# Kernel tuning notes

Measured on AMD Instinct MI355X. Metric: run time of the kernel, lower is better.

Reference implementation:

```python
import jax, jax.numpy as jnp
import numpy as np

N = 10000
IN_DIM = 1024
HID = 128
LAT = 64
E = 320000


def setup_inputs() -> dict:
    key = jax.random.key(0)
    ks = jax.random.split(key, 12)
    def glorot(k, shape):
        lim = float(np.sqrt(6.0 / (shape[0] + shape[1])))
        return jax.random.uniform(k, shape, jnp.float32, -lim, lim)
    x = jax.random.normal(ks[0], (N, IN_DIM), jnp.float32)
    edge_index = jax.random.randint(ks[1], (2, E), 0, N, jnp.int64)
    return {
        "x": x,
        "edge_index": edge_index,
        "W_enc1": glorot(ks[2], (IN_DIM, HID)), "b_enc1": jnp.zeros((HID,), jnp.float32),
        "W_enc2": glorot(ks[3], (HID, LAT)),   "b_enc2": jnp.zeros((LAT,), jnp.float32),
        "W_att1": glorot(ks[4], (LAT, HID)),   "b_att1": jnp.zeros((HID,), jnp.float32),
        "W_att2": glorot(ks[5], (HID, IN_DIM)),"b_att2": jnp.zeros((IN_DIM,), jnp.float32),
        "W_str":  glorot(ks[6], (LAT, LAT)),   "b_str":  jnp.zeros((LAT,), jnp.float32),
    }


def _gcn_norm(edge_index, n):
    # PyG GCNConv default: add self-loops, symmetric normalization
    loop = jnp.arange(n, dtype=edge_index.dtype)
    send = jnp.concatenate([edge_index[0], loop])
    recv = jnp.concatenate([edge_index[1], loop])
    deg = jax.ops.segment_sum(jnp.ones_like(recv, dtype=jnp.float32), recv, num_segments=n)
    dis = jnp.where(deg > 0, jax.lax.rsqrt(deg), 0.0)
    norm = dis[send] * dis[recv]  # [E+N]
    return send, recv, norm


def _gcn(x, W, b, send, recv, norm, n):
    h = x @ W                                  # [N, out]
    msg = h[send] * norm[:, None]              # gather + scale
    agg = jax.ops.segment_sum(msg, recv, num_segments=n)  # scatter-add
    return agg + b


def reference(x, edge_index, W_enc1, b_enc1, W_enc2, b_enc2,
              W_att1, b_att1, W_att2, b_att2, W_str, b_str):
    n = x.shape[0]
    send, recv, norm = _gcn_norm(edge_index, n)
    # encoder
    h = jax.nn.relu(_gcn(x, W_enc1, b_enc1, send, recv, norm, n))
    z = jax.nn.relu(_gcn(h, W_enc2, b_enc2, send, recv, norm, n))
    # attribute decoder
    a = jax.nn.relu(_gcn(z, W_att1, b_att1, send, recv, norm, n))
    attr_recon = jax.nn.relu(_gcn(a, W_att2, b_att2, send, recv, norm, n))
    # structure decoder
    s = jax.nn.relu(_gcn(z, W_str, b_str, send, recv, norm, n))
    struct_recon = s @ s.T  # [N, N]
    return (attr_recon, struct_recon, z)
```

## Files before the change

### kernel.cpp

```cpp
#include <hip/hip_runtime.h>
#include <hip/hip_bf16.h>

#define IN_DIM 1024
#define HID 128
#define LAT 64
#define DEGPAD 128

typedef __attribute__((ext_vector_type(8))) short bf16x8;
typedef __attribute__((ext_vector_type(4))) short bf16x4;
typedef __attribute__((ext_vector_type(4))) float f32x4;


__global__ __launch_bounds__(256) void k_initcur(int* cursor, int n) {
    int i = blockIdx.x * 256 + threadIdx.x;
    if (i < n) cursor[i] = 0;
}

__global__ __launch_bounds__(256) void k_fillpad(const int* __restrict__ ei, int* cursor,
                                                 int* __restrict__ colPad, int E) {
    int e = blockIdx.x * 256 + threadIdx.x;
    if (e >= E) return;
    int s = ei[e], r = ei[E + e];
    int slot = atomicAdd(&cursor[r], 1);
    if (slot < DEGPAD) colPad[(size_t)r * DEGPAD + slot] = s;
}

__global__ __launch_bounds__(256) void k_dis(const int* __restrict__ cursor, float* dis, int n) {
    int i = blockIdx.x * 256 + threadIdx.x;
    if (i < n) dis[i] = rsqrtf((float)(cursor[i] + 1));
}


#define W1T_OFF 0
#define W2T_OFF 131072
#define Wa1T_OFF 139264
#define Wa2T_OFF 147456
#define WsT_OFF 278528
#define WT_TOTAL 282624

__global__ __launch_bounds__(256) void k_wsplit(const float* __restrict__ W1, const float* __restrict__ W2,
                                                const float* __restrict__ Wa1, const float* __restrict__ Wa2,
                                                const float* __restrict__ Ws,
                                                __hip_bfloat16* __restrict__ hi, __hip_bfloat16* __restrict__ lo) {
    int idx = blockIdx.x * 256 + threadIdx.x;
    if (idx >= WT_TOTAL) return;
    const float* src; int base, shK, Nc;
    if (idx < W2T_OFF)       { src = W1;  base = W1T_OFF;  shK = 10; Nc = 128; }
    else if (idx < Wa1T_OFF) { src = W2;  base = W2T_OFF;  shK = 7;  Nc = 64; }
    else if (idx < Wa2T_OFF) { src = Wa1; base = Wa1T_OFF; shK = 6;  Nc = 128; }
    else if (idx < WsT_OFF)  { src = Wa2; base = Wa2T_OFF; shK = 7;  Nc = 1024; }
    else                     { src = Ws;  base = WsT_OFF;  shK = 6;  Nc = 64; }
    int local = idx - base;
    int nn = local >> shK;
    int k = local & ((1 << shK) - 1);
    float v = src[(size_t)k * Nc + nn];
    __hip_bfloat16 h = __float2bfloat16(v);
    hi[idx] = h;
    lo[idx] = __float2bfloat16(v - __bfloat162float(h));
}


template<int F, bool BIAS, bool RELU, int OMODE>
__global__ __launch_bounds__(256) void k_spmm(const float* __restrict__ Hin,
                                              const int* __restrict__ colPad,
                                              const int* __restrict__ cursor,
                                              const float* __restrict__ dis,
                                              const float* __restrict__ bias,
                                              float* __restrict__ out, float* __restrict__ out2,
                                              __hip_bfloat16* __restrict__ ohi,
                                              __hip_bfloat16* __restrict__ olo, int n) {
    int wave = (blockIdx.x * 256 + threadIdx.x) >> 6;
    int lane = threadIdx.x & 63;
    if (wave >= n) return;
    int d = cursor[wave];
    if (d > DEGPAD) d = DEGPAD;
    const int* cp = colPad + (size_t)wave * DEGPAD;
    float acc[F / 64];
    const float* self = Hin + (size_t)wave * F;
#pragma unroll
    for (int j = 0; j < F / 64; ++j) acc[j] = self[lane + 64 * j];
    for (int p = 0; p < d; ++p) {
        int c = cp[p];
        const float* row = Hin + (size_t)c * F;
#pragma unroll
        for (int j = 0; j < F / 64; ++j) acc[j] += row[lane + 64 * j];
    }
    float di = dis[wave];
#pragma unroll
    for (int j = 0; j < F / 64; ++j) {
        float r = acc[j] * di;
        if (BIAS) r += bias[lane + 64 * j];
        if (RELU) r = fmaxf(r, 0.f);
        size_t idx = (size_t)wave * F + lane + 64 * j;
        if constexpr (OMODE == 1) {
            __hip_bfloat16 h = __float2bfloat16(r);
            ohi[idx] = h;
            olo[idx] = __float2bfloat16(r - __bfloat162float(h));
        } else {
            out[idx] = r;
            if constexpr (OMODE == 2) out2[idx] = r * di;
        }
    }
}


template<int AMODE, bool BIAS, bool RELU, bool DIS, bool SPLITOUT, bool NT>
__global__ __launch_bounds__(256) void k_gemm_mfma(
        const __hip_bfloat16* __restrict__ Ahi, const __hip_bfloat16* __restrict__ Alo,
        const float* __restrict__ Af,
        const __hip_bfloat16* __restrict__ Bthi, const __hip_bfloat16* __restrict__ Btlo,
        const float* __restrict__ bias, const float* __restrict__ dis,
        float* __restrict__ Cf, __hip_bfloat16* __restrict__ Chi, __hip_bfloat16* __restrict__ Clo,
        int M, int K, int Nc) {
    __shared__ float tile[128 * 68];
    int tid = threadIdx.x;
    int w = tid >> 6, lane = tid & 63;
    int wr = w >> 1, wc = w & 1;
    int m0 = blockIdx.y * 128, n0 = blockIdx.x * 64;
    int lrow = lane & 15, lk = (lane >> 4) * 8;

    int arow[4];
    size_t aoff[4];
#pragma unroll
    for (int mi = 0; mi < 4; ++mi) {
        arow[mi] = m0 + wr * 64 + mi * 16 + lrow;
        aoff[mi] = (size_t)arow[mi] * K + lk;
    }
    size_t boff[2];
#pragma unroll
    for (int nj = 0; nj < 2; ++nj)
        boff[nj] = (size_t)(n0 + wc * 32 + nj * 16 + lrow) * K + lk;

    f32x4 acc[4][2] = {};

    for (int k0 = 0; k0 < K; k0 += 32) {
        bf16x8 bh[2], bl[2], ah[4], al[4];
#pragma unroll
        for (int nj = 0; nj < 2; ++nj) {
            bh[nj] = *(const bf16x8*)(Bthi + boff[nj] + k0);
            bl[nj] = *(const bf16x8*)(Btlo + boff[nj] + k0);
        }
        if constexpr (AMODE == 0) {
#pragma unroll
            for (int mi = 0; mi < 4; ++mi) {
                ah[mi] = *(const bf16x8*)(Ahi + aoff[mi] + k0);
                al[mi] = *(const bf16x8*)(Alo + aoff[mi] + k0);
            }
        } else {
#pragma unroll
            for (int mi = 0; mi < 4; ++mi) {
                float4 f0 = make_float4(0.f, 0.f, 0.f, 0.f), f1 = f0;
                if (arow[mi] < M) {
                    f0 = *(const float4*)(Af + aoff[mi] + k0);
                    f1 = *(const float4*)(Af + aoff[mi] + k0 + 4);
                }
                float ff[8] = {f0.x, f0.y, f0.z, f0.w, f1.x, f1.y, f1.z, f1.w};
                __attribute__((aligned(16))) __hip_bfloat16 hb[8], lb[8];
#pragma unroll
                for (int t = 0; t < 8; ++t) {
                    __hip_bfloat16 h = __float2bfloat16(ff[t]);
                    hb[t] = h;
                    lb[t] = __float2bfloat16(ff[t] - __bfloat162float(h));
                }
                ah[mi] = *(const bf16x8*)hb;
                al[mi] = *(const bf16x8*)lb;
            }
        }
#pragma unroll
        for (int mi = 0; mi < 4; ++mi)
#pragma unroll
            for (int nj = 0; nj < 2; ++nj) {
                acc[mi][nj] = __builtin_amdgcn_mfma_f32_16x16x32_bf16(ah[mi], bh[nj], acc[mi][nj], 0, 0, 0);
                acc[mi][nj] = __builtin_amdgcn_mfma_f32_16x16x32_bf16(ah[mi], bl[nj], acc[mi][nj], 0, 0, 0);
                acc[mi][nj] = __builtin_amdgcn_mfma_f32_16x16x32_bf16(al[mi], bh[nj], acc[mi][nj], 0, 0, 0);
            }
    }

    int r0 = (lane >> 4) * 4;
#pragma unroll
    for (int mi = 0; mi < 4; ++mi)
#pragma unroll
        for (int nj = 0; nj < 2; ++nj) {
            int cl = wc * 32 + nj * 16 + lrow;
#pragma unroll
            for (int r = 0; r < 4; ++r) {
                int rl = wr * 64 + mi * 16 + r0 + r;
                tile[rl * 68 + cl] = acc[mi][nj][r];
            }
        }
    __syncthreads();

#pragma unroll
    for (int it = 0; it < 8; ++it) {
        int rl = it * 16 + (tid >> 4);
        int c4 = tid & 15;
        int row = m0 + rl;
        if (row >= M) continue;
        int col = n0 + c4 * 4;
        float4 v = *(const float4*)&tile[rl * 68 + c4 * 4];
        if (BIAS) {
            float4 b = *(const float4*)&bias[col];
            v.x += b.x; v.y += b.y; v.z += b.z; v.w += b.w;
        }
        if (RELU) {
            v.x = fmaxf(v.x, 0.f); v.y = fmaxf(v.y, 0.f);
            v.z = fmaxf(v.z, 0.f); v.w = fmaxf(v.w, 0.f);
        }
        if (DIS) {
            float di = dis[row];
            v.x *= di; v.y *= di; v.z *= di; v.w *= di;
        }
        if constexpr (SPLITOUT) {
            float vv[4] = {v.x, v.y, v.z, v.w};
            __attribute__((aligned(8))) __hip_bfloat16 hs[4], ls[4];
#pragma unroll
            for (int k = 0; k < 4; ++k) {
                hs[k] = __float2bfloat16(vv[k]);
                ls[k] = __float2bfloat16(vv[k] - __bfloat162float(hs[k]));
            }
            *(bf16x4*)&Chi[(size_t)row * Nc + col] = *(bf16x4*)hs;
            *(bf16x4*)&Clo[(size_t)row * Nc + col] = *(bf16x4*)ls;
        } else if constexpr (NT) {
            __builtin_nontemporal_store(*(const f32x4*)&v, (f32x4*)&Cf[(size_t)row * Nc + col]);
        } else {
            *(float4*)&Cf[(size_t)row * Nc + col] = v;
        }
    }
}


__device__ __forceinline__ int swz(int rl, int c4) { return (c4 ^ (rl & 31)); }

__global__ __launch_bounds__(256) void k_sst_mfma(const __hip_bfloat16* __restrict__ Shi,
                                                  const __hip_bfloat16* __restrict__ Slo,
                                                  float* __restrict__ C, int M) {
    int bx = blockIdx.x, by = blockIdx.y;
    if (by < bx) return;
    __shared__ float tile[128 * 128];

    int w = threadIdx.x >> 6, lane = threadIdx.x & 63;
    int wr = w >> 1, wc = w & 1;
    int i0 = bx * 128 + wr * 64;
    int j0 = by * 128 + wc * 64;
    int lrow = lane & 15;
    int lk = (lane >> 4) * 8;

    f32x4 acc[4][4] = {};

#pragma unroll
    for (int ks = 0; ks < 2; ++ks) {
        bf16x8 ah[4], al[4], bh[4], bl[4];
#pragma unroll
        for (int mi = 0; mi < 4; ++mi) {
            size_t off = (size_t)(i0 + mi * 16 + lrow) * 64 + ks * 32 + lk;
            ah[mi] = *(const bf16x8*)(Shi + off);
            al[mi] = *(const bf16x8*)(Slo + off);
        }
#pragma unroll
        for (int nj = 0; nj < 4; ++nj) {
            size_t off = (size_t)(j0 + nj * 16 + lrow) * 64 + ks * 32 + lk;
            bh[nj] = *(const bf16x8*)(Shi + off);
            bl[nj] = *(const bf16x8*)(Slo + off);
        }
#pragma unroll
        for (int mi = 0; mi < 4; ++mi)
#pragma unroll
            for (int nj = 0; nj < 4; ++nj) {
                acc[mi][nj] = __builtin_amdgcn_mfma_f32_16x16x32_bf16(ah[mi], bh[nj], acc[mi][nj], 0, 0, 0);
                acc[mi][nj] = __builtin_amdgcn_mfma_f32_16x16x32_bf16(ah[mi], bl[nj], acc[mi][nj], 0, 0, 0);
                acc[mi][nj] = __builtin_amdgcn_mfma_f32_16x16x32_bf16(al[mi], bh[nj], acc[mi][nj], 0, 0, 0);
            }
    }

    int r0 = (lane >> 4) * 4;
#pragma unroll
    for (int mi = 0; mi < 4; ++mi)
#pragma unroll
        for (int nj = 0; nj < 4; ++nj) {
#pragma unroll
            for (int r = 0; r < 4; ++r) {
                int rl = wr * 64 + mi * 16 + r0 + r;
                int cl = wc * 64 + nj * 16 + lrow;
                tile[rl * 128 + (swz(rl, cl >> 2) << 2) + (cl & 3)] = acc[mi][nj][r];
            }
        }
    __syncthreads();

    int i0b = bx * 128, j0b = by * 128;
    int tt = threadIdx.x;

#pragma unroll
    for (int it = 0; it < 16; ++it) {
        int rl = it * 8 + (tt >> 5);
        int c4 = tt & 31;
        int row = i0b + rl;
        if (row >= M) continue;
        int col = j0b + c4 * 4;
        if (col >= M) continue;
        float4 v = *(const float4*)&tile[rl * 128 + (swz(rl, c4) << 2)];
        if (col + 3 < M) {
            __builtin_nontemporal_store(*(const f32x4*)&v, (f32x4*)&C[(size_t)row * M + col]);
        } else {
            float vv[4] = {v.x, v.y, v.z, v.w};
            for (int k = 0; k < 4 && col + k < M; ++k) C[(size_t)row * M + col + k] = vv[k];
        }
    }

    if (bx != by) {
#pragma unroll
        for (int it = 0; it < 16; ++it) {
            int cl = it * 8 + (tt >> 5);
            int row = j0b + cl;
            if (row >= M) continue;
            int rbase = (tt & 31) * 4;
            int col = i0b + rbase;
            if (col >= M) continue;
            float vv[4];
#pragma unroll
            for (int k = 0; k < 4; ++k) {
                int rr = rbase + k;
                vv[k] = tile[rr * 128 + (swz(rr, cl >> 2) << 2) + (cl & 3)];
            }
            if (col + 3 < M) {
                float4 v = make_float4(vv[0], vv[1], vv[2], vv[3]);
                __builtin_nontemporal_store(*(const f32x4*)&v, (f32x4*)&C[(size_t)row * M + col]);
            } else {
                for (int k = 0; k < 4 && col + k < M; ++k) C[(size_t)row * M + col + k] = vv[k];
            }
        }
    }
}


extern "C" void kernel_launch(void* const* d_in, const int* in_sizes, int n_in,
                              void* d_out, int out_size, void* d_ws, size_t ws_size,
                              hipStream_t stream) {
    const float* x   = (const float*)d_in[0];
    const int*   ei  = (const int*)d_in[1];
    const float* W1  = (const float*)d_in[2];
    const float* b1  = (const float*)d_in[3];
    const float* W2  = (const float*)d_in[4];
    const float* b2  = (const float*)d_in[5];
    const float* Wa1 = (const float*)d_in[6];
    const float* ba1 = (const float*)d_in[7];
    const float* Wa2 = (const float*)d_in[8];
    const float* ba2 = (const float*)d_in[9];
    const float* Ws  = (const float*)d_in[10];
    const float* bs  = (const float*)d_in[11];

    int N = in_sizes[0] / IN_DIM;
    int E = in_sizes[1] / 2;
    int Mpad = ((N + 127) / 128) * 128;

    float* out  = (float*)d_out;
    float* attr = out;
    float* st   = out + (size_t)N * IN_DIM;
    float* zout = st + (size_t)N * N;

    char* basep = (char*)d_ws;
    size_t off = 0;
    auto alloc = [&](size_t bytes) -> void* {
        void* p = basep + off;
        off = (off + bytes + 255) & ~(size_t)255;
        return p;
    };

    int*   colPad = (int*)alloc((size_t)N * DEGPAD * 4);
    int*   cursor = (int*)alloc((size_t)N * 4);
    float* dis    = (float*)alloc((size_t)N * 4);
    __hip_bfloat16* Whi = (__hip_bfloat16*)alloc((size_t)WT_TOTAL * 2);
    __hip_bfloat16* Wlo = (__hip_bfloat16*)alloc((size_t)WT_TOTAL * 2);
    float* t128 = (float*)alloc((size_t)N * 128 * 4);
    float* t64  = (float*)alloc((size_t)N * 64 * 4);
    float* zp   = (float*)alloc((size_t)N * 64 * 4);
    __hip_bfloat16* Hhi  = (__hip_bfloat16*)alloc((size_t)Mpad * 128 * 2);
    __hip_bfloat16* Hlo  = (__hip_bfloat16*)alloc((size_t)Mpad * 128 * 2);
    __hip_bfloat16* AZhi = (__hip_bfloat16*)alloc((size_t)Mpad * 64 * 2);
    __hip_bfloat16* AZlo = (__hip_bfloat16*)alloc((size_t)Mpad * 64 * 2);
    __hip_bfloat16* AAhi = (__hip_bfloat16*)alloc((size_t)Mpad * 128 * 2);
    __hip_bfloat16* AAlo = (__hip_bfloat16*)alloc((size_t)Mpad * 128 * 2);
    __hip_bfloat16* Shi  = (__hip_bfloat16*)alloc((size_t)Mpad * 64 * 2);
    __hip_bfloat16* Slo  = (__hip_bfloat16*)alloc((size_t)Mpad * 64 * 2);

    dim3 b256(256);
    int nb_n = (N + 255) / 256;
    int spmm_grid = (N * 64 + 255) / 256;

    k_initcur<<<dim3(nb_n), b256, 0, stream>>>(cursor, N);
    k_wsplit<<<dim3((WT_TOTAL + 255) / 256), b256, 0, stream>>>(W1, W2, Wa1, Wa2, Ws, Whi, Wlo);
    k_fillpad<<<dim3((E + 255) / 256), b256, 0, stream>>>(ei, cursor, colPad, E);
    k_dis<<<dim3(nb_n), b256, 0, stream>>>(cursor, dis, N);

    k_gemm_mfma<1, false, false, true, false, false><<<dim3(2, Mpad / 128), b256, 0, stream>>>(
        nullptr, nullptr, x, Whi + W1T_OFF, Wlo + W1T_OFF, nullptr, dis,
        t128, nullptr, nullptr, N, 1024, 128);
    k_spmm<128, true, true, 1><<<dim3(spmm_grid), b256, 0, stream>>>(
        t128, colPad, cursor, dis, b1, nullptr, nullptr, Hhi, Hlo, N);
    k_gemm_mfma<0, false, false, true, false, false><<<dim3(1, Mpad / 128), b256, 0, stream>>>(
        Hhi, Hlo, nullptr, Whi + W2T_OFF, Wlo + W2T_OFF, nullptr, dis,
        t64, nullptr, nullptr, N, 128, 64);
    k_spmm<64, true, true, 2><<<dim3(spmm_grid), b256, 0, stream>>>(
        t64, colPad, cursor, dis, b2, zout, zp, nullptr, nullptr, N);
    k_spmm<64, false, false, 1><<<dim3(spmm_grid), b256, 0, stream>>>(
        zp, colPad, cursor, dis, nullptr, nullptr, nullptr, AZhi, AZlo, N);
    k_gemm_mfma<0, true, true, true, false, false><<<dim3(2, Mpad / 128), b256, 0, stream>>>(
        AZhi, AZlo, nullptr, Whi + Wa1T_OFF, Wlo + Wa1T_OFF, ba1, dis,
        t128, nullptr, nullptr, N, 64, 128);
    k_spmm<128, false, false, 1><<<dim3(spmm_grid), b256, 0, stream>>>(
        t128, colPad, cursor, dis, nullptr, nullptr, nullptr, AAhi, AAlo, N);
    k_gemm_mfma<0, true, true, false, false, true><<<dim3(16, Mpad / 128), b256, 0, stream>>>(
        AAhi, AAlo, nullptr, Whi + Wa2T_OFF, Wlo + Wa2T_OFF, ba2, nullptr,
        attr, nullptr, nullptr, N, 128, 1024);
    k_gemm_mfma<0, true, true, false, true, false><<<dim3(1, Mpad / 128), b256, 0, stream>>>(
        AZhi, AZlo, nullptr, Whi + WsT_OFF, Wlo + WsT_OFF, bs, nullptr,
        nullptr, Shi, Slo, N, 64, 64);
    k_sst_mfma<<<dim3(Mpad / 128, Mpad / 128), b256, 0, stream>>>(Shi, Slo, st, N);
}
```

Measured before the change: 367.8 us.

## Fuse all GCN stages into one cooperative persistent kernel with grid syncs

Replaces the chain of separate kernel launches with a single persistent cooperative kernel that runs nine phases separated by grid-wide barriers, falling back to per-phase launches if cooperative launch fails. The degree normalisation is now recomputed inside the SpMM from the cursor counts instead of being stored in a separate array. Independent GEMMs share a phase: Wa1 with Ws, and Wa2 with the S·Sᵀ product, which now uses smaller 128x64 tiles sized to the shared smem buffer. The aim is to remove launch gaps and tail idling, at the cost of grid-sync overhead, a fixed grid size, and an extra gather of neighbour degrees inside the SpMM.

```diff
diff --git a/kernel.cpp b/kernel.cpp
--- a/kernel.cpp
+++ b/kernel.cpp
@@ -1,4 +1,5 @@
 #include <hip/hip_runtime.h>
+#include <hip/hip_cooperative_groups.h>
 #include <hip/hip_bf16.h>
 
 #define IN_DIM 1024
@@ -9,27 +10,6 @@
 typedef __attribute__((ext_vector_type(8))) short bf16x8;
 typedef __attribute__((ext_vector_type(4))) short bf16x4;
 typedef __attribute__((ext_vector_type(4))) float f32x4;
-
-
-__global__ __launch_bounds__(256) void k_initcur(int* cursor, int n) {
-    int i = blockIdx.x * 256 + threadIdx.x;
-    if (i < n) cursor[i] = 0;
-}
-
-__global__ __launch_bounds__(256) void k_fillpad(const int* __restrict__ ei, int* cursor,
-                                                 int* __restrict__ colPad, int E) {
-    int e = blockIdx.x * 256 + threadIdx.x;
-    if (e >= E) return;
-    int s = ei[e], r = ei[E + e];
-    int slot = atomicAdd(&cursor[r], 1);
-    if (slot < DEGPAD) colPad[(size_t)r * DEGPAD + slot] = s;
-}
-
-__global__ __launch_bounds__(256) void k_dis(const int* __restrict__ cursor, float* dis, int n) {
-    int i = blockIdx.x * 256 + threadIdx.x;
-    if (i < n) dis[i] = rsqrtf((float)(cursor[i] + 1));
-}
-
 
 #define W1T_OFF 0
 #define W2T_OFF 131072
@@ -38,85 +18,41 @@
 #define WsT_OFF 278528
 #define WT_TOTAL 282624
 
-__global__ __launch_bounds__(256) void k_wsplit(const float* __restrict__ W1, const float* __restrict__ W2,
-                                                const float* __restrict__ Wa1, const float* __restrict__ Wa2,
-                                                const float* __restrict__ Ws,
-                                                __hip_bfloat16* __restrict__ hi, __hip_bfloat16* __restrict__ lo) {
-    int idx = blockIdx.x * 256 + threadIdx.x;
-    if (idx >= WT_TOTAL) return;
-    const float* src; int base, shK, Nc;
-    if (idx < W2T_OFF)       { src = W1;  base = W1T_OFF;  shK = 10; Nc = 128; }
-    else if (idx < Wa1T_OFF) { src = W2;  base = W2T_OFF;  shK = 7;  Nc = 64; }
-    else if (idx < Wa2T_OFF) { src = Wa1; base = Wa1T_OFF; shK = 6;  Nc = 128; }
-    else if (idx < WsT_OFF)  { src = Wa2; base = Wa2T_OFF; shK = 7;  Nc = 1024; }
-    else                     { src = Ws;  base = WsT_OFF;  shK = 6;  Nc = 64; }
-    int local = idx - base;
-    int nn = local >> shK;
-    int k = local & ((1 << shK) - 1);
-    float v = src[(size_t)k * Nc + nn];
-    __hip_bfloat16 h = __float2bfloat16(v);
-    hi[idx] = h;
-    lo[idx] = __float2bfloat16(v - __bfloat162float(h));
-}
-
-
-template<int F, bool BIAS, bool RELU, int OMODE>
-__global__ __launch_bounds__(256) void k_spmm(const float* __restrict__ Hin,
-                                              const int* __restrict__ colPad,
-                                              const int* __restrict__ cursor,
-                                              const float* __restrict__ dis,
-                                              const float* __restrict__ bias,
-                                              float* __restrict__ out, float* __restrict__ out2,
-                                              __hip_bfloat16* __restrict__ ohi,
-                                              __hip_bfloat16* __restrict__ olo, int n) {
-    int wave = (blockIdx.x * 256 + threadIdx.x) >> 6;
-    int lane = threadIdx.x & 63;
-    if (wave >= n) return;
-    int d = cursor[wave];
-    if (d > DEGPAD) d = DEGPAD;
-    const int* cp = colPad + (size_t)wave * DEGPAD;
-    float acc[F / 64];
-    const float* self = Hin + (size_t)wave * F;
-#pragma unroll
-    for (int j = 0; j < F / 64; ++j) acc[j] = self[lane + 64 * j];
-    for (int p = 0; p < d; ++p) {
-        int c = cp[p];
-        const float* row = Hin + (size_t)c * F;
-#pragma unroll
-        for (int j = 0; j < F / 64; ++j) acc[j] += row[lane + 64 * j];
-    }
-    float di = dis[wave];
-#pragma unroll
-    for (int j = 0; j < F / 64; ++j) {
-        float r = acc[j] * di;
-        if (BIAS) r += bias[lane + 64 * j];
-        if (RELU) r = fmaxf(r, 0.f);
-        size_t idx = (size_t)wave * F + lane + 64 * j;
-        if constexpr (OMODE == 1) {
-            __hip_bfloat16 h = __float2bfloat16(r);
-            ohi[idx] = h;
-            olo[idx] = __float2bfloat16(r - __bfloat162float(h));
-        } else {
-            out[idx] = r;
-            if constexpr (OMODE == 2) out2[idx] = r * di;
-        }
-    }
-}
-
-
-template<int AMODE, bool BIAS, bool RELU, bool DIS, bool SPLITOUT, bool NT>
-__global__ __launch_bounds__(256) void k_gemm_mfma(
+struct MegaArgs {
+    const float* x; const int* ei;
+    const float* W1; const float* b1; const float* W2; const float* b2;
+    const float* Wa1; const float* ba1; const float* Wa2; const float* ba2;
+    const float* Ws; const float* bs;
+    float* attr; float* st; float* zout;
+    int* colPad; int* cursor;
+    __hip_bfloat16* Whi; __hip_bfloat16* Wlo;
+    float* t128; float* t64;
+    __hip_bfloat16* Hhi; __hip_bfloat16* Hlo;
+    __hip_bfloat16* AZhi; __hip_bfloat16* AZlo;
+    __hip_bfloat16* AAhi; __hip_bfloat16* AAlo;
+    __hip_bfloat16* Shi; __hip_bfloat16* Slo;
+    int N; int E; int Mpad;
+    int coop; int ph_lo; int ph_hi;
+};
+
+__device__ __forceinline__ void splitf(float v, __hip_bfloat16& h, __hip_bfloat16& l) {
+    h = __float2bfloat16(v);
+    l = __float2bfloat16(v - __bfloat162float(h));
+}
+
+
+template<int AMODE, bool BIAS, bool RELU, bool SPLITOUT, bool NT>
+__device__ void dev_gemm(float* smem, int bx, int byy,
         const __hip_bfloat16* __restrict__ Ahi, const __hip_bfloat16* __restrict__ Alo,
         const float* __restrict__ Af,
         const __hip_bfloat16* __restrict__ Bthi, const __hip_bfloat16* __restrict__ Btlo,
-        const float* __restrict__ bias, const float* __restrict__ dis,
+        const float* __restrict__ bias,
         float* __restrict__ Cf, __hip_bfloat16* __restrict__ Chi, __hip_bfloat16* __restrict__ Clo,
         int M, int K, int Nc) {
-    __shared__ float tile[128 * 68];
     int tid = threadIdx.x;
     int w = tid >> 6, lane = tid & 63;
     int wr = w >> 1, wc = w & 1;
-    int m0 = blockIdx.y * 128, n0 = blockIdx.x * 64;
+    int m0 = byy * 128, n0 = bx * 64;
     int lrow = lane & 15, lk = (lane >> 4) * 8;
 
     int arow[4];
@@ -157,11 +93,7 @@
                 float ff[8] = {f0.x, f0.y, f0.z, f0.w, f1.x, f1.y, f1.z, f1.w};
                 __attribute__((aligned(16))) __hip_bfloat16 hb[8], lb[8];
 #pragma unroll
-                for (int t = 0; t < 8; ++t) {
-                    __hip_bfloat16 h = __float2bfloat16(ff[t]);
-                    hb[t] = h;
-                    lb[t] = __float2bfloat16(ff[t] - __bfloat162float(h));
-                }
+                for (int t = 0; t < 8; ++t) splitf(ff[t], hb[t], lb[t]);
                 ah[mi] = *(const bf16x8*)hb;
                 al[mi] = *(const bf16x8*)lb;
             }
@@ -185,7 +117,7 @@
 #pragma unroll
             for (int r = 0; r < 4; ++r) {
                 int rl = wr * 64 + mi * 16 + r0 + r;
-                tile[rl * 68 + cl] = acc[mi][nj][r];
+                smem[rl * 68 + cl] = acc[mi][nj][r];
             }
         }
     __syncthreads();
@@ -195,61 +127,93 @@
         int rl = it * 16 + (tid >> 4);
         int c4 = tid & 15;
         int row = m0 + rl;
-        if (row >= M) continue;
-        int col = n0 + c4 * 4;
-        float4 v = *(const float4*)&tile[rl * 68 + c4 * 4];
-        if (BIAS) {
-            float4 b = *(const float4*)&bias[col];
-            v.x += b.x; v.y += b.y; v.z += b.z; v.w += b.w;
-        }
-        if (RELU) {
-            v.x = fmaxf(v.x, 0.f); v.y = fmaxf(v.y, 0.f);
-            v.z = fmaxf(v.z, 0.f); v.w = fmaxf(v.w, 0.f);
-        }
-        if (DIS) {
-            float di = dis[row];
-            v.x *= di; v.y *= di; v.z *= di; v.w *= di;
-        }
-        if constexpr (SPLITOUT) {
-            float vv[4] = {v.x, v.y, v.z, v.w};
-            __attribute__((aligned(8))) __hip_bfloat16 hs[4], ls[4];
-#pragma unroll
-            for (int k = 0; k < 4; ++k) {
-                hs[k] = __float2bfloat16(vv[k]);
-                ls[k] = __float2bfloat16(vv[k] - __bfloat162float(hs[k]));
-            }
-            *(bf16x4*)&Chi[(size_t)row * Nc + col] = *(bf16x4*)hs;
-            *(bf16x4*)&Clo[(size_t)row * Nc + col] = *(bf16x4*)ls;
-        } else if constexpr (NT) {
-            __builtin_nontemporal_store(*(const f32x4*)&v, (f32x4*)&Cf[(size_t)row * Nc + col]);
-        } else {
-            *(float4*)&Cf[(size_t)row * Nc + col] = v;
-        }
-    }
-}
-
-
-__device__ __forceinline__ int swz(int rl, int c4) { return (c4 ^ (rl & 31)); }
-
-__global__ __launch_bounds__(256) void k_sst_mfma(const __hip_bfloat16* __restrict__ Shi,
-                                                  const __hip_bfloat16* __restrict__ Slo,
-                                                  float* __restrict__ C, int M) {
-    int bx = blockIdx.x, by = blockIdx.y;
-    if (by < bx) return;
-    __shared__ float tile[128 * 128];
-
-    int w = threadIdx.x >> 6, lane = threadIdx.x & 63;
+        if (row < M) {
+            int col = n0 + c4 * 4;
+            float4 v = *(const float4*)&smem[rl * 68 + c4 * 4];
+            if (BIAS) {
+                float4 b = *(const float4*)&bias[col];
+                v.x += b.x; v.y += b.y; v.z += b.z; v.w += b.w;
+            }
+            if (RELU) {
+                v.x = fmaxf(v.x, 0.f); v.y = fmaxf(v.y, 0.f);
+                v.z = fmaxf(v.z, 0.f); v.w = fmaxf(v.w, 0.f);
+            }
+            if constexpr (SPLITOUT) {
+                float vv[4] = {v.x, v.y, v.z, v.w};
+                __attribute__((aligned(8))) __hip_bfloat16 hs[4], ls[4];
+#pragma unroll
+                for (int k = 0; k < 4; ++k) splitf(vv[k], hs[k], ls[k]);
+                *(bf16x4*)&Chi[(size_t)row * Nc + col] = *(bf16x4*)hs;
+                *(bf16x4*)&Clo[(size_t)row * Nc + col] = *(bf16x4*)ls;
+            } else if constexpr (NT) {
+                __builtin_nontemporal_store(*(const f32x4*)&v, (f32x4*)&Cf[(size_t)row * Nc + col]);
+            } else {
+                *(float4*)&Cf[(size_t)row * Nc + col] = v;
+            }
+        }
+    }
+    __syncthreads();
+}
+
+
+template<int F, bool BIAS, bool RELU, int OMODE>
+__device__ void dev_spmm(const float* __restrict__ Hin,
+                         const int* __restrict__ colPad, const int* __restrict__ cursor,
+                         const float* __restrict__ bias,
+                         float* __restrict__ out,
+                         __hip_bfloat16* __restrict__ ohi, __hip_bfloat16* __restrict__ olo,
+                         int n) {
+    int gw = (blockIdx.x * 256 + threadIdx.x) >> 6;
+    int nw = (gridDim.x * 256) >> 6;
+    int lane = threadIdx.x & 63;
+    for (int i = gw; i < n; i += nw) {
+        int d = cursor[i];
+        float di = rsqrtf((float)(d + 1));
+        if (d > DEGPAD) d = DEGPAD;
+        const int* cp = colPad + (size_t)i * DEGPAD;
+        float acc[F / 64];
+        const float* self = Hin + (size_t)i * F;
+#pragma unroll
+        for (int j = 0; j < F / 64; ++j) acc[j] = di * self[lane + 64 * j];
+        for (int p = 0; p < d; ++p) {
+            int c = cp[p];
+            float dc = rsqrtf((float)(cursor[c] + 1));
+            const float* row = Hin + (size_t)c * F;
+#pragma unroll
+            for (int j = 0; j < F / 64; ++j) acc[j] = fmaf(dc, row[lane + 64 * j], acc[j]);
+        }
+#pragma unroll
+        for (int j = 0; j < F / 64; ++j) {
+            float r = acc[j] * di;
+            if (BIAS) r += bias[lane + 64 * j];
+            if (RELU) r = fmaxf(r, 0.f);
+            size_t idx = (size_t)i * F + lane + 64 * j;
+            if constexpr (OMODE == 1) {
+                __hip_bfloat16 h, l;
+                splitf(r, h, l);
+                ohi[idx] = h; olo[idx] = l;
+            } else {
+                out[idx] = r;
+            }
+        }
+    }
+}
+
+
+__device__ void dev_sst(float* smem, int bi, int bj64,
+                        const __hip_bfloat16* __restrict__ Shi, const __hip_bfloat16* __restrict__ Slo,
+                        float* __restrict__ C, int M) {
+    int tid = threadIdx.x;
+    int w = tid >> 6, lane = tid & 63;
     int wr = w >> 1, wc = w & 1;
-    int i0 = bx * 128 + wr * 64;
-    int j0 = by * 128 + wc * 64;
-    int lrow = lane & 15;
-    int lk = (lane >> 4) * 8;
-
-    f32x4 acc[4][4] = {};
-
+    int I = bi * 128, J = bj64 * 64;
+    int i0 = I + wr * 64, j0 = J + wc * 32;
+    int lrow = lane & 15, lk = (lane >> 4) * 8;
+
+    f32x4 acc[4][2] = {};
 #pragma unroll
     for (int ks = 0; ks < 2; ++ks) {
-        bf16x8 ah[4], al[4], bh[4], bl[4];
+        bf16x8 ah[4], al[4], bh[2], bl[2];
 #pragma unroll
         for (int mi = 0; mi < 4; ++mi) {
             size_t off = (size_t)(i0 + mi * 16 + lrow) * 64 + ks * 32 + lk;
@@ -257,7 +221,7 @@
             al[mi] = *(const bf16x8*)(Slo + off);
         }
 #pragma unroll
-        for (int nj = 0; nj < 4; ++nj) {
+        for (int nj = 0; nj < 2; ++nj) {
             size_t off = (size_t)(j0 + nj * 16 + lrow) * 64 + ks * 32 + lk;
             bh[nj] = *(const bf16x8*)(Shi + off);
             bl[nj] = *(const bf16x8*)(Slo + off);
@@ -265,7 +229,7 @@
 #pragma unroll
         for (int mi = 0; mi < 4; ++mi)
 #pragma unroll
-            for (int nj = 0; nj < 4; ++nj) {
+            for (int nj = 0; nj < 2; ++nj) {
                 acc[mi][nj] = __builtin_amdgcn_mfma_f32_16x16x32_bf16(ah[mi], bh[nj], acc[mi][nj], 0, 0, 0);
                 acc[mi][nj] = __builtin_amdgcn_mfma_f32_16x16x32_bf16(ah[mi], bl[nj], acc[mi][nj], 0, 0, 0);
                 acc[mi][nj] = __builtin_amdgcn_mfma_f32_16x16x32_bf16(al[mi], bh[nj], acc[mi][nj], 0, 0, 0);
@@ -276,58 +240,140 @@
 #pragma unroll
     for (int mi = 0; mi < 4; ++mi)
 #pragma unroll
-        for (int nj = 0; nj < 4; ++nj) {
+        for (int nj = 0; nj < 2; ++nj) {
+            int cl = wc * 32 + nj * 16 + lrow;
 #pragma unroll
             for (int r = 0; r < 4; ++r) {
                 int rl = wr * 64 + mi * 16 + r0 + r;
-                int cl = wc * 64 + nj * 16 + lrow;
-                tile[rl * 128 + (swz(rl, cl >> 2) << 2) + (cl & 3)] = acc[mi][nj][r];
+                int c4s = (cl >> 2) ^ (rl & 15);
+                smem[rl * 68 + (c4s << 2) + (cl & 3)] = acc[mi][nj][r];
             }
         }
     __syncthreads();
 
-    int i0b = bx * 128, j0b = by * 128;
-    int tt = threadIdx.x;
-
-#pragma unroll
-    for (int it = 0; it < 16; ++it) {
-        int rl = it * 8 + (tt >> 5);
-        int c4 = tt & 31;
-        int row = i0b + rl;
-        if (row >= M) continue;
-        int col = j0b + c4 * 4;
-        if (col >= M) continue;
-        float4 v = *(const float4*)&tile[rl * 128 + (swz(rl, c4) << 2)];
-        if (col + 3 < M) {
+#pragma unroll
+    for (int it = 0; it < 8; ++it) {
+        int rl = it * 16 + (tid >> 4);
+        int c4 = tid & 15;
+        int row = I + rl, col = J + c4 * 4;
+        if (row < M && col < M) {
+            int c4s = c4 ^ (rl & 15);
+            float4 v = *(const float4*)&smem[rl * 68 + (c4s << 2)];
             __builtin_nontemporal_store(*(const f32x4*)&v, (f32x4*)&C[(size_t)row * M + col]);
-        } else {
-            float vv[4] = {v.x, v.y, v.z, v.w};
-            for (int k = 0; k < 4 && col + k < M; ++k) C[(size_t)row * M + col + k] = vv[k];
-        }
-    }
-
-    if (bx != by) {
-#pragma unroll
-        for (int it = 0; it < 16; ++it) {
-            int cl = it * 8 + (tt >> 5);
-            int row = j0b + cl;
-            if (row >= M) continue;
-            int rbase = (tt & 31) * 4;
-            int col = i0b + rbase;
-            if (col >= M) continue;
-            float vv[4];
-#pragma unroll
-            for (int k = 0; k < 4; ++k) {
-                int rr = rbase + k;
-                vv[k] = tile[rr * 128 + (swz(rr, cl >> 2) << 2) + (cl & 3)];
-            }
-            if (col + 3 < M) {
+        }
+    }
+    if (bj64 >= 2 * bi + 2) {
+#pragma unroll
+        for (int it = 0; it < 8; ++it) {
+            int cl = it * 8 + (tid >> 5);
+            int rbase = (tid & 31) * 4;
+            int row = J + cl, col = I + rbase;
+            if (row < M && col < M) {
+                float vv[4];
+#pragma unroll
+                for (int k = 0; k < 4; ++k) {
+                    int rr = rbase + k;
+                    vv[k] = smem[rr * 68 + ((((cl >> 2) ^ (rr & 15))) << 2) + (cl & 3)];
+                }
                 float4 v = make_float4(vv[0], vv[1], vv[2], vv[3]);
                 __builtin_nontemporal_store(*(const f32x4*)&v, (f32x4*)&C[(size_t)row * M + col]);
-            } else {
-                for (int k = 0; k < 4 && col + k < M; ++k) C[(size_t)row * M + col + k] = vv[k];
-            }
-        }
+            }
+        }
+    }
+    __syncthreads();
+}
+
+
+__device__ void run_phase(int ph, const MegaArgs& A, float* smem) {
+    int gtid = blockIdx.x * 256 + threadIdx.x;
+    int gsz = gridDim.x * 256;
+    int nt = A.Mpad / 128;
+    switch (ph) {
+    case 0: {
+        for (int i = gtid; i < A.N; i += gsz) A.cursor[i] = 0;
+        for (int idx = gtid; idx < WT_TOTAL; idx += gsz) {
+            const float* src; int base, shK, Nc;
+            if (idx < W2T_OFF)       { src = A.W1;  base = W1T_OFF;  shK = 10; Nc = 128; }
+            else if (idx < Wa1T_OFF) { src = A.W2;  base = W2T_OFF;  shK = 7;  Nc = 64; }
+            else if (idx < Wa2T_OFF) { src = A.Wa1; base = Wa1T_OFF; shK = 6;  Nc = 128; }
+            else if (idx < WsT_OFF)  { src = A.Wa2; base = Wa2T_OFF; shK = 7;  Nc = 1024; }
+            else                     { src = A.Ws;  base = WsT_OFF;  shK = 6;  Nc = 64; }
+            int local = idx - base;
+            int nn = local >> shK;
+            int k = local & ((1 << shK) - 1);
+            splitf(src[(size_t)k * Nc + nn], A.Whi[idx], A.Wlo[idx]);
+        }
+        break;
+    }
+    case 1: {
+        for (int e = gtid; e < A.E; e += gsz) {
+            int s = A.ei[e], r = A.ei[A.E + e];
+            int slot = atomicAdd(&A.cursor[r], 1);
+            if (slot < DEGPAD) A.colPad[(size_t)r * DEGPAD + slot] = s;
+        }
+        for (int t = blockIdx.x; t < 2 * nt; t += gridDim.x)
+            dev_gemm<1, false, false, false, false>(smem, t & 1, t >> 1,
+                nullptr, nullptr, A.x, A.Whi + W1T_OFF, A.Wlo + W1T_OFF, nullptr,
+                A.t128, nullptr, nullptr, A.N, 1024, 128);
+        break;
+    }
+    case 2:
+        dev_spmm<128, true, true, 1>(A.t128, A.colPad, A.cursor, A.b1, nullptr, A.Hhi, A.Hlo, A.N);
+        break;
+    case 3:
+        for (int t = blockIdx.x; t < nt; t += gridDim.x)
+            dev_gemm<0, false, false, false, false>(smem, 0, t,
+                A.Hhi, A.Hlo, nullptr, A.Whi + W2T_OFF, A.Wlo + W2T_OFF, nullptr,
+                A.t64, nullptr, nullptr, A.N, 128, 64);
+        break;
+    case 4:
+        dev_spmm<64, true, true, 0>(A.t64, A.colPad, A.cursor, A.b2, A.zout, nullptr, nullptr, A.N);
+        break;
+    case 5:
+        dev_spmm<64, false, false, 1>(A.zout, A.colPad, A.cursor, nullptr, nullptr, A.AZhi, A.AZlo, A.N);
+        break;
+    case 6: {
+        int n3 = 2 * nt;
+        for (int t = blockIdx.x; t < n3 + nt; t += gridDim.x) {
+            if (t < n3)
+                dev_gemm<0, true, true, false, false>(smem, t & 1, t >> 1,
+                    A.AZhi, A.AZlo, nullptr, A.Whi + Wa1T_OFF, A.Wlo + Wa1T_OFF, A.ba1,
+                    A.t128, nullptr, nullptr, A.N, 64, 128);
+            else
+                dev_gemm<0, true, true, true, false>(smem, 0, t - n3,
+                    A.AZhi, A.AZlo, nullptr, A.Whi + WsT_OFF, A.Wlo + WsT_OFF, A.bs,
+                    nullptr, A.Shi, A.Slo, A.N, 64, 64);
+        }
+        break;
+    }
+    case 7:
+        dev_spmm<128, false, false, 1>(A.t128, A.colPad, A.cursor, nullptr, nullptr, A.AAhi, A.AAlo, A.N);
+        break;
+    case 8: {
+        int nG5 = 16 * nt;
+        int nSST = nt * (nt + 1);
+        for (int t = blockIdx.x; t < nG5 + nSST; t += gridDim.x) {
+            if (t < nG5)
+                dev_gemm<0, true, true, false, true>(smem, t & 15, t >> 4,
+                    A.AAhi, A.AAlo, nullptr, A.Whi + Wa2T_OFF, A.Wlo + Wa2T_OFF, A.ba2,
+                    A.attr, nullptr, nullptr, A.N, 128, 1024);
+            else {
+                int tt = t - nG5;
+                int bi = 0;
+                while (tt >= 2 * (nt - bi)) { tt -= 2 * (nt - bi); bi++; }
+                dev_sst(smem, bi, 2 * bi + tt, A.Shi, A.Slo, A.st, A.N);
+            }
+        }
+        break;
+    }
+    }
+}
+
+__global__ __launch_bounds__(256, 2) void k_mega(MegaArgs A) {
+    __shared__ float smem[128 * 68];
+    for (int ph = A.ph_lo; ph <= A.ph_hi; ++ph) {
+        run_phase(ph, A, smem);
+        if (A.coop && ph != A.ph_hi) cooperative_groups::this_grid().sync();
     }
 }
 
@@ -335,27 +381,23 @@
 extern "C" void kernel_launch(void* const* d_in, const int* in_sizes, int n_in,
                               void* d_out, int out_size, void* d_ws, size_t ws_size,
                               hipStream_t stream) {
-    const float* x   = (const float*)d_in[0];
-    const int*   ei  = (const int*)d_in[1];
-    const float* W1  = (const float*)d_in[2];
-    const float* b1  = (const float*)d_in[3];
-    const float* W2  = (const float*)d_in[4];
-    const float* b2  = (const float*)d_in[5];
-    const float* Wa1 = (const float*)d_in[6];
-    const float* ba1 = (const float*)d_in[7];
-    const float* Wa2 = (const float*)d_in[8];
-    const float* ba2 = (const float*)d_in[9];
-    const float* Ws  = (const float*)d_in[10];
-    const float* bs  = (const float*)d_in[11];
-
-    int N = in_sizes[0] / IN_DIM;
-    int E = in_sizes[1] / 2;
-    int Mpad = ((N + 127) / 128) * 128;
-
-    float* out  = (float*)d_out;
-    float* attr = out;
-    float* st   = out + (size_t)N * IN_DIM;
-    float* zout = st + (size_t)N * N;
+    MegaArgs A;
+    A.x   = (const float*)d_in[0];
+    A.ei  = (const int*)d_in[1];
+    A.W1  = (const float*)d_in[2];  A.b1  = (const float*)d_in[3];
+    A.W2  = (const float*)d_in[4];  A.b2  = (const float*)d_in[5];
+    A.Wa1 = (const float*)d_in[6];  A.ba1 = (const float*)d_in[7];
+    A.Wa2 = (const float*)d_in[8];  A.ba2 = (const float*)d_in[9];
+    A.Ws  = (const float*)d_in[10]; A.bs  = (const float*)d_in[11];
+
+    A.N = in_sizes[0] / IN_DIM;
+    A.E = in_sizes[1] / 2;
+    A.Mpad = ((A.N + 127) / 128) * 128;
+
+    float* out = (float*)d_out;
+    A.attr = out;
+    A.st   = out + (size_t)A.N * IN_DIM;
+    A.zout = A.st + (size_t)A.N * A.N;
 
     char* basep = (char*)d_ws;
     size_t off = 0;
@@ -364,55 +406,39 @@
         off = (off + bytes + 255) & ~(size_t)255;
         return p;
     };
-
-    int*   colPad = (int*)alloc((size_t)N * DEGPAD * 4);
-    int*   cursor = (int*)alloc((size_t)N * 4);
-    float* dis    = (float*)alloc((size_t)N * 4);
-    __hip_bfloat16* Whi = (__hip_bfloat16*)alloc((size_t)WT_TOTAL * 2);
-    __hip_bfloat16* Wlo = (__hip_bfloat16*)alloc((size_t)WT_TOTAL * 2);
-    float* t128 = (float*)alloc((size_t)N * 128 * 4);
-    float* t64  = (float*)alloc((size_t)N * 64 * 4);
-    float* zp   = (float*)alloc((size_t)N * 64 * 4);
-    __hip_bfloat16* Hhi  = (__hip_bfloat16*)alloc((size_t)Mpad * 128 * 2);
-    __hip_bfloat16* Hlo  = (__hip_bfloat16*)alloc((size_t)Mpad * 128 * 2);
-    __hip_bfloat16* AZhi = (__hip_bfloat16*)alloc((size_t)Mpad * 64 * 2);
-    __hip_bfloat16* AZlo = (__hip_bfloat16*)alloc((size_t)Mpad * 64 * 2);
-    __hip_bfloat16* AAhi = (__hip_bfloat16*)alloc((size_t)Mpad * 128 * 2);
-    __hip_bfloat16* AAlo = (__hip_bfloat16*)alloc((size_t)Mpad * 128 * 2);
-    __hip_bfloat16* Shi  = (__hip_bfloat16*)alloc((size_t)Mpad * 64 * 2);
-    __hip_bfloat16* Slo  = (__hip_bfloat16*)alloc((size_t)Mpad * 64 * 2);
-
-    dim3 b256(256);
-    int nb_n = (N + 255) / 256;
-    int spmm_grid = (N * 64 + 255) / 256;
-
-    k_initcur<<<dim3(nb_n), b256, 0, stream>>>(cursor, N);
-    k_wsplit<<<dim3((WT_TOTAL + 255) / 256), b256, 0, stream>>>(W1, W2, Wa1, Wa2, Ws, Whi, Wlo);
-    k_fillpad<<<dim3((E + 255) / 256), b256, 0, stream>>>(ei, cursor, colPad, E);
-    k_dis<<<dim3(nb_n), b256, 0, stream>>>(cursor, dis, N);
-
-    k_gemm_mfma<1, false, false, true, false, false><<<dim3(2, Mpad / 128), b256, 0, stream>>>(
-        nullptr, nullptr, x, Whi + W1T_OFF, Wlo + W1T_OFF, nullptr, dis,
-        t128, nullptr, nullptr, N, 1024, 128);
-    k_spmm<128, true, true, 1><<<dim3(spmm_grid), b256, 0, stream>>>(
-        t128, colPad, cursor, dis, b1, nullptr, nullptr, Hhi, Hlo, N);
-    k_gemm_mfma<0, false, false, true, false, false><<<dim3(1, Mpad / 128), b256, 0, stream>>>(
-        Hhi, Hlo, nullptr, Whi + W2T_OFF, Wlo + W2T_OFF, nullptr, dis,
-        t64, nullptr, nullptr, N, 128, 64);
-    k_spmm<64, true, true, 2><<<dim3(spmm_grid), b256, 0, stream>>>(
-        t64, colPad, cursor, dis, b2, zout, zp, nullptr, nullptr, N);
-    k_spmm<64, false, false, 1><<<dim3(spmm_grid), b256, 0, stream>>>(
-        zp, colPad, cursor, dis, nullptr, nullptr, nullptr, AZhi, AZlo, N);
-    k_gemm_mfma<0, true, true, true, false, false><<<dim3(2, Mpad / 128), b256, 0, stream>>>(
-        AZhi, AZlo, nullptr, Whi + Wa1T_OFF, Wlo + Wa1T_OFF, ba1, dis,
-        t128, nullptr, nullptr, N, 64, 128);
-    k_spmm<128, false, false, 1><<<dim3(spmm_grid), b256, 0, stream>>>(
-        t128, colPad, cursor, dis, nullptr, nullptr, nullptr, AAhi, AAlo, N);
-    k_gemm_mfma<0, true, true, false, false, true><<<dim3(16, Mpad / 128), b256, 0, stream>>>(
-        AAhi, AAlo, nullptr, Whi + Wa2T_OFF, Wlo + Wa2T_OFF, ba2, nullptr,
-        attr, nullptr, nullptr, N, 128, 1024);
-    k_gemm_mfma<0, true, true, false, true, false><<<dim3(1, Mpad / 128), b256, 0, stream>>>(
-        AZhi, AZlo, nullptr, Whi + WsT_OFF, Wlo + WsT_OFF, bs, nullptr,
-        nullptr, Shi, Slo, N, 64, 64);
-    k_sst_mfma<<<dim3(Mpad / 128, Mpad / 128), b256, 0, stream>>>(Shi, Slo, st, N);
-}
+    A.colPad = (int*)alloc((size_t)A.N * DEGPAD * 4);
+    A.cursor = (int*)alloc((size_t)A.N * 4);
+    A.Whi = (__hip_bfloat16*)alloc((size_t)WT_TOTAL * 2);
+    A.Wlo = (__hip_bfloat16*)alloc((size_t)WT_TOTAL * 2);
+    A.t128 = (float*)alloc((size_t)A.N * 128 * 4);
+    A.t64  = (float*)alloc((size_t)A.N * 64 * 4);
+    A.Hhi  = (__hip_bfloat16*)alloc((size_t)A.Mpad * 128 * 2);
+    A.Hlo  = (__hip_bfloat16*)alloc((size_t)A.Mpad * 128 * 2);
+    A.AZhi = (__hip_bfloat16*)alloc((size_t)A.Mpad * 64 * 2);
+    A.AZlo = (__hip_bfloat16*)alloc((size_t)A.Mpad * 64 * 2);
+    A.AAhi = (__hip_bfloat16*)alloc((size_t)A.Mpad * 128 * 2);
+    A.AAlo = (__hip_bfloat16*)alloc((size_t)A.Mpad * 128 * 2);
+    A.Shi  = (__hip_bfloat16*)alloc((size_t)A.Mpad * 64 * 2);
+    A.Slo  = (__hip_bfloat16*)alloc((size_t)A.Mpad * 64 * 2);
+
+    int dev = 0;
+    hipGetDevice(&dev);
+    int ncu = 256;
+    hipDeviceGetAttribute(&ncu, hipDeviceAttributeMultiprocessorCount, dev);
+    int maxb = 0;
+    hipOccupancyMaxActiveBlocksPerMultiprocessor(&maxb, k_mega, 256, 0);
+    if (maxb < 1) maxb = 1;
+    int grid = ncu * maxb;
+
+    A.coop = 1; A.ph_lo = 0; A.ph_hi = 8;
+    void* kargs[] = { (void*)&A };
+    hipError_t err = hipLaunchCooperativeKernel((const void*)k_mega, dim3(grid), dim3(256),
+                                                kargs, 0, stream);
+    if (err != hipSuccess) {
+        for (int p = 0; p <= 8; ++p) {
+            MegaArgs B = A;
+            B.coop = 0; B.ph_lo = B.ph_hi = p;
+            k_mega<<<dim3(grid), dim3(256), 0, stream>>>(B);
+        }
+    }
+}
```

Result: slower. 1.010 ms (+174.7%).
